# Optimization experiments

Measured on AMD Instinct MI355X. Metric: run time of the kernel, lower is better.

The kernel has to match this reference:

```python
import jax, jax.numpy as jnp
import numpy as np

B, H, N, F = 64, 24, 32, 256

def setup_inputs() -> dict:
    key = jax.random.key(0)
    ks = jax.random.split(key, 6)
    s = 1.0 / np.sqrt(F)
    return {
        "Q": jax.random.normal(ks[0], (B, N, F), jnp.float32),
        "K": jax.random.normal(ks[1], (B, H, N, F), jnp.float32),
        "V": jax.random.normal(ks[2], (B, H, N, F), jnp.float32),
        "Wq": jax.random.normal(ks[3], (N, F, F), jnp.float32) * s,
        "bq": jnp.zeros((N, F), jnp.float32),
        "Wk": jax.random.normal(ks[4], (N, H, F, F), jnp.float32) * s,
        "bk": jnp.zeros((N, H, F), jnp.float32),
        "Wv": jax.random.normal(ks[5], (N, H, F, F), jnp.float32) * s,
        "bv": jnp.zeros((N, H, F), jnp.float32),
    }

def reference(Q, K, V, Wq, bq, Wk, bk, Wv, bv):
    # Per-node query projection: [B,N,F]
    QWq = jnp.einsum('bnf,nfg->bng', Q, Wq) + bq
    # Per-node, per-encoder-step key/value projections: [B,N,H,F]
    KWk = jnp.einsum('bhnf,nhfg->bnhg', K, Wk) + bk
    VWv = jnp.einsum('bhnf,nhfg->bnhg', V, Wv) + bv
    # Attention scores over the H encoder steps (no sqrt(F) scaling, as in source)
    logits = jnp.einsum('bng,bnhg->bnh', QWq, KWk)
    scores = jax.nn.softmax(logits, axis=-1)          # [B,N,H]
    heads = jnp.einsum('bnh,bnhg->bng', scores, VWv)  # [B,N,F]
    return heads, scores
```

## Files before the change

### kernel.cpp

```cpp
#include <hip/hip_runtime.h>

typedef __attribute__((ext_vector_type(8))) short short8;
typedef __attribute__((ext_vector_type(4))) float f32x4;

#define B_ 64
#define H_ 24
#define N_ 32
#define F_ 256

__device__ __forceinline__ float bf2f(unsigned short u) {
    return __uint_as_float(((unsigned)u) << 16);
}
__device__ __forceinline__ unsigned short f2bf(float f) {
    unsigned u = __float_as_uint(f);
    u += 0x7fffu + ((u >> 16) & 1u);
    return (unsigned short)(u >> 16);
}
__device__ __forceinline__ unsigned pack_hi(float f0, float f1) {
    return (__float_as_uint(f0) >> 16) | (__float_as_uint(f1) & 0xffff0000u);
}
__device__ __forceinline__ float res_lo(float f) {
    return f - __uint_as_float(__float_as_uint(f) & 0xffff0000u);
}

struct StageT {
    unsigned short Ah[64 * 32];
    unsigned short Al[64 * 32];
    unsigned short Wh[256 * 32];
    unsigned short Wl[256 * 32];
};
union Smem {
    StageT t;
    unsigned short outT[64 * 256];
};

template<bool SPLIT>
__device__ __forceinline__ void gemm_f32(
    const float* __restrict__ Ab, long rstride,
    const float* __restrict__ Wb, Smem& sm, f32x4 acc[4][4])
{
    const int t    = threadIdx.x;
    const int lane = t & 63;
    const int wv   = t >> 6;
    const int l15  = lane & 15;
    const int quad = lane >> 4;
    const int arow = t >> 2, achk = (t & 3) * 8;
    const float* aSrc = Ab + (long)arow * rstride + achk;
    const float* wSrc = Wb + (long)(wv * 8) * 256 + lane * 4;
    const int pos  = wv ^ (lane & 3);
    const int bpos = quad ^ ((l15 >> 2) & 3);

    union F4 { float4 v; float e[4]; };

    float4 a0 = *(const float4*)(aSrc);
    float4 a1 = *(const float4*)(aSrc + 4);
    F4 r[8];
    #pragma unroll
    for (int i = 0; i < 8; i++) r[i].v = *(const float4*)(wSrc + i * 256);

    #pragma unroll
    for (int ks = 0; ks < 8; ks++) {
        __syncthreads();
        {
            uint4 h;
            h.x = pack_hi(a0.x, a0.y); h.y = pack_hi(a0.z, a0.w);
            h.z = pack_hi(a1.x, a1.y); h.w = pack_hi(a1.z, a1.w);
            *(uint4*)&sm.t.Ah[arow * 32 + achk] = h;
            if (SPLIT) {
                uint4 l;
                l.x = pack_hi(res_lo(a0.x), res_lo(a0.y));
                l.y = pack_hi(res_lo(a0.z), res_lo(a0.w));
                l.z = pack_hi(res_lo(a1.x), res_lo(a1.y));
                l.w = pack_hi(res_lo(a1.z), res_lo(a1.w));
                *(uint4*)&sm.t.Al[arow * 32 + achk] = l;
            }
            #pragma unroll
            for (int j = 0; j < 4; j++) {
                uint4 hh;
                hh.x = pack_hi(r[0].e[j], r[1].e[j]);
                hh.y = pack_hi(r[2].e[j], r[3].e[j]);
                hh.z = pack_hi(r[4].e[j], r[5].e[j]);
                hh.w = pack_hi(r[6].e[j], r[7].e[j]);
                *(uint4*)&sm.t.Wh[(lane * 4 + j) * 32 + pos * 8] = hh;
                if (SPLIT) {
                    uint4 ll;
                    ll.x = pack_hi(res_lo(r[0].e[j]), res_lo(r[1].e[j]));
                    ll.y = pack_hi(res_lo(r[2].e[j]), res_lo(r[3].e[j]));
                    ll.z = pack_hi(res_lo(r[4].e[j]), res_lo(r[5].e[j]));
                    ll.w = pack_hi(res_lo(r[6].e[j]), res_lo(r[7].e[j]));
                    *(uint4*)&sm.t.Wl[(lane * 4 + j) * 32 + pos * 8] = ll;
                }
            }
        }
        __syncthreads();
        float4 na0, na1;
        F4 nr[8];
        if (ks < 7) {
            const int k1 = (ks + 1) * 32;
            na0 = *(const float4*)(aSrc + k1);
            na1 = *(const float4*)(aSrc + k1 + 4);
            #pragma unroll
            for (int i = 0; i < 8; i++)
                nr[i].v = *(const float4*)(wSrc + k1 * 256 + i * 256);
        }
        {
            short8 ah[4];
            #pragma unroll
            for (int mi = 0; mi < 4; mi++)
                ah[mi] = *(const short8*)&sm.t.Ah[(mi * 16 + l15) * 32 + quad * 8];
            if (SPLIT) {
                short8 al[4];
                #pragma unroll
                for (int mi = 0; mi < 4; mi++)
                    al[mi] = *(const short8*)&sm.t.Al[(mi * 16 + l15) * 32 + quad * 8];
                #pragma unroll
                for (int ni = 0; ni < 4; ni++) {
                    int g = wv * 64 + ni * 16 + l15;
                    short8 bh = *(const short8*)&sm.t.Wh[g * 32 + bpos * 8];
                    short8 bl = *(const short8*)&sm.t.Wl[g * 32 + bpos * 8];
                    #pragma unroll
                    for (int mi = 0; mi < 4; mi++) {
                        acc[mi][ni] = __builtin_amdgcn_mfma_f32_16x16x32_bf16(al[mi], bh, acc[mi][ni], 0, 0, 0);
                        acc[mi][ni] = __builtin_amdgcn_mfma_f32_16x16x32_bf16(ah[mi], bl, acc[mi][ni], 0, 0, 0);
                        acc[mi][ni] = __builtin_amdgcn_mfma_f32_16x16x32_bf16(ah[mi], bh, acc[mi][ni], 0, 0, 0);
                    }
                }
            } else {
                #pragma unroll
                for (int ni = 0; ni < 4; ni++) {
                    int g = wv * 64 + ni * 16 + l15;
                    short8 bh = *(const short8*)&sm.t.Wh[g * 32 + bpos * 8];
                    #pragma unroll
                    for (int mi = 0; mi < 4; mi++)
                        acc[mi][ni] = __builtin_amdgcn_mfma_f32_16x16x32_bf16(ah[mi], bh, acc[mi][ni], 0, 0, 0);
                }
            }
        }
        a0 = na0; a1 = na1;
        #pragma unroll
        for (int i = 0; i < 8; i++) r[i] = nr[i];
    }
}

__global__ __launch_bounds__(256, 3) void k_qproj(
    const float* __restrict__ Q, const float* __restrict__ Wq,
    const float* __restrict__ bq, float* __restrict__ qws)
{
    const int n = blockIdx.x;
    __shared__ Smem sm;
    f32x4 acc[4][4];
    #pragma unroll
    for (int i = 0; i < 4; i++)
        #pragma unroll
        for (int j = 0; j < 4; j++) acc[i][j] = (f32x4){0.f, 0.f, 0.f, 0.f};

    gemm_f32<true>(Q + n * F_, (long)(N_ * F_), Wq + (long)n * F_ * F_, sm, acc);

    const int t = threadIdx.x, lane = t & 63, wv = t >> 6;
    const int l15 = lane & 15, quad = lane >> 4;
    const float* bias = bq + n * F_;
    float* dst = qws + (long)n * (B_ * F_);
    #pragma unroll
    for (int ni = 0; ni < 4; ni++) {
        int g = wv * 64 + ni * 16 + l15;
        float bb = bias[g];
        #pragma unroll
        for (int mi = 0; mi < 4; mi++)
            #pragma unroll
            for (int reg = 0; reg < 4; reg++) {
                int r = mi * 16 + quad * 4 + reg;
                dst[r * 256 + g] = acc[mi][ni][reg] + bb;
            }
    }
}

__global__ __launch_bounds__(256, 3) void k_kvproj(
    const float* __restrict__ Kx, const float* __restrict__ Vx,
    const float* __restrict__ Wk, const float* __restrict__ bk,
    const float* __restrict__ Wv, const float* __restrict__ bv,
    const float* __restrict__ qws, float* __restrict__ logits,
    unsigned short* __restrict__ vws)
{
    const int nh = blockIdx.x;
    const int n = nh / H_;
    const int h = nh - n * H_;
    const bool isV = (blockIdx.y != 0);
    const float* X    = isV ? Vx : Kx;
    const float* W    = (isV ? Wv : Wk) + (long)nh * F_ * F_;
    const float* bias = (isV ? bv : bk) + nh * F_;

    __shared__ Smem sm;
    __shared__ float slog[64];
    const int t = threadIdx.x;
    if (!isV && t < 64) slog[t] = 0.f;

    f32x4 acc[4][4];
    #pragma unroll
    for (int i = 0; i < 4; i++)
        #pragma unroll
        for (int j = 0; j < 4; j++) acc[i][j] = (f32x4){0.f, 0.f, 0.f, 0.f};

    const float* Xb = X + (long)(h * N_ + n) * F_;
    if (isV) gemm_f32<false>(Xb, (long)(H_ * N_ * F_), W, sm, acc);
    else     gemm_f32<true >(Xb, (long)(H_ * N_ * F_), W, sm, acc);

    const int lane = t & 63, wv = t >> 6, l15 = lane & 15, quad = lane >> 4;

    if (!isV) {
        const float* qrow = qws + (long)n * (B_ * F_);
        #pragma unroll
        for (int mi = 0; mi < 4; mi++) {
            float p[4] = {0.f, 0.f, 0.f, 0.f};
            #pragma unroll
            for (int ni = 0; ni < 4; ni++) {
                int g = wv * 64 + ni * 16 + l15;
                float bb = bias[g];
                #pragma unroll
                for (int reg = 0; reg < 4; reg++) {
                    int r = mi * 16 + quad * 4 + reg;
                    p[reg] += (acc[mi][ni][reg] + bb) * qrow[r * 256 + g];
                }
            }
            #pragma unroll
            for (int off = 1; off < 16; off <<= 1)
                #pragma unroll
                for (int reg = 0; reg < 4; reg++)
                    p[reg] += __shfl_xor(p[reg], off, 64);
            if (l15 == 0)
                #pragma unroll
                for (int reg = 0; reg < 4; reg++)
                    atomicAdd(&slog[mi * 16 + quad * 4 + reg], p[reg]);
        }
        __syncthreads();
        if (t < 64) logits[(long)nh * 64 + t] = slog[t];
    } else {
        __syncthreads();
        #pragma unroll
        for (int ni = 0; ni < 4; ni++) {
            int g = wv * 64 + ni * 16 + l15;
            float bb = bias[g];
            #pragma unroll
            for (int mi = 0; mi < 4; mi++)
                #pragma unroll
                for (int reg = 0; reg < 4; reg++) {
                    int r = mi * 16 + quad * 4 + reg;
                    sm.outT[r * 256 + g] = f2bf(acc[mi][ni][reg] + bb);
                }
        }
        __syncthreads();
        unsigned short* dst = vws + (long)nh * (B_ * F_);
        #pragma unroll
        for (int it = 0; it < 8; it++) {
            int row = it * 8 + (t >> 5);
            int c = t & 31;
            uint4 v = *(const uint4*)(&sm.outT[row * 256 + c * 8]);
            *(uint4*)(dst + row * 256 + c * 8) = v;
        }
    }
}

__global__ __launch_bounds__(64) void k_attn(
    const float* __restrict__ logits,
    const unsigned short* __restrict__ vws,
    float* __restrict__ out)
{
    const int bx = blockIdx.x;
    const int b = bx >> 5;
    const int n = bx & 31;
    const int t = threadIdx.x;
    __shared__ float sl[24], se[24];
    if (t < 24) sl[t] = logits[(long)(n * H_ + t) * 64 + b];
    __syncthreads();
    float mx = -1e30f;
    #pragma unroll
    for (int h = 0; h < H_; h++) mx = fmaxf(mx, sl[h]);
    if (t < 24) se[t] = expf(sl[t] - mx);
    __syncthreads();
    float den = 0.f;
    #pragma unroll
    for (int h = 0; h < H_; h++) den += se[h];
    float inv = 1.0f / den;
    if (t < 24)
        out[(long)B_ * N_ * F_ + (long)(b * N_ + n) * H_ + t] = se[t] * inv;

    const int g0 = t * 4;
    float hv[4] = {0.f, 0.f, 0.f, 0.f};
    #pragma unroll
    for (int h = 0; h < H_; h++) {
        float s = se[h] * inv;
        const unsigned short* vp = vws + (((long)(n * H_ + h) * 64 + b) << 8) + g0;
        union { uint2 u; unsigned short e[4]; } vv;
        vv.u = *(const uint2*)vp;
        #pragma unroll
        for (int j = 0; j < 4; j++) hv[j] += s * bf2f(vv.e[j]);
    }
    float4 ov = make_float4(hv[0], hv[1], hv[2], hv[3]);
    *(float4*)(out + ((long)b * N_ + n) * F_ + g0) = ov;
}

extern "C" void kernel_launch(void* const* d_in, const int* in_sizes, int n_in,
                              void* d_out, int out_size, void* d_ws, size_t ws_size,
                              hipStream_t stream) {
    const float* Q  = (const float*)d_in[0];
    const float* K  = (const float*)d_in[1];
    const float* V  = (const float*)d_in[2];
    const float* Wq = (const float*)d_in[3];
    const float* bq = (const float*)d_in[4];
    const float* Wk = (const float*)d_in[5];
    const float* bk = (const float*)d_in[6];
    const float* Wv = (const float*)d_in[7];
    const float* bv = (const float*)d_in[8];

    char* ws = (char*)d_ws;
    float* qws          = (float*)ws;
    float* logits       = (float*)(ws + 2097152);
    unsigned short* vws = (unsigned short*)(ws + 2097152 + 262144);

    k_qproj<<<N_, 256, 0, stream>>>(Q, Wq, bq, qws);
    k_kvproj<<<dim3(N_ * H_, 2), 256, 0, stream>>>(K, V, Wk, bk, Wv, bv, qws, logits, vws);
    k_attn<<<B_ * N_, 64, 0, stream>>>(logits, vws, (float*)d_out);
}
```

Before: 496.4 us.

## Split Q projection over K with atomics and restructure GEMM prefetch barriers

The Q projection now launches 8× more blocks, one per 32-wide K-slice, and accumulates partial results into a pre-zeroed workspace with atomicAdd. A separate zeroing kernel runs first. The GEMM loop issues the next global loads before the LDS write stage and replaces __syncthreads with explicit lgkmcnt waits plus s_barrier. It also raises occupancy hints to 4 blocks per CU and reuses shared memory for the logit scratch. The aim is to fix the 32-block underutilization of the Q projection and to overlap global loads with LDS conversion, at the cost of an extra launch, atomic traffic and nondeterministic summation order.

```diff
diff --git a/kernel.cpp b/kernel.cpp
--- a/kernel.cpp
+++ b/kernel.cpp
@@ -37,7 +37,8 @@
 template<bool SPLIT>
 __device__ __forceinline__ void gemm_f32(
     const float* __restrict__ Ab, long rstride,
-    const float* __restrict__ Wb, Smem& sm, f32x4 acc[4][4])
+    const float* __restrict__ Wb, Smem& sm, f32x4 acc[4][4],
+    int ksBeg, int ksEnd)
 {
     const int t    = threadIdx.x;
     const int lane = t & 63;
@@ -52,15 +53,28 @@
 
     union F4 { float4 v; float e[4]; };
 
-    float4 a0 = *(const float4*)(aSrc);
-    float4 a1 = *(const float4*)(aSrc + 4);
+    float4 a0 = *(const float4*)(aSrc + ksBeg * 32);
+    float4 a1 = *(const float4*)(aSrc + ksBeg * 32 + 4);
     F4 r[8];
     #pragma unroll
-    for (int i = 0; i < 8; i++) r[i].v = *(const float4*)(wSrc + i * 256);
-
-    #pragma unroll
-    for (int ks = 0; ks < 8; ks++) {
-        __syncthreads();
+    for (int i = 0; i < 8; i++)
+        r[i].v = *(const float4*)(wSrc + (long)(ksBeg * 32 + i) * 256);
+
+    for (int ks = ksBeg; ks < ksEnd; ks++) {
+        asm volatile("s_waitcnt lgkmcnt(0)" ::: "memory");
+        __builtin_amdgcn_s_barrier();
+
+        float4 na0, na1;
+        F4 nr[8];
+        if (ks + 1 < ksEnd) {
+            const int k1 = (ks + 1) * 32;
+            na0 = *(const float4*)(aSrc + k1);
+            na1 = *(const float4*)(aSrc + k1 + 4);
+            #pragma unroll
+            for (int i = 0; i < 8; i++)
+                nr[i].v = *(const float4*)(wSrc + (long)(k1 + i) * 256);
+        }
+
         {
             uint4 h;
             h.x = pack_hi(a0.x, a0.y); h.y = pack_hi(a0.z, a0.w);
@@ -92,17 +106,9 @@
                 }
             }
         }
-        __syncthreads();
-        float4 na0, na1;
-        F4 nr[8];
-        if (ks < 7) {
-            const int k1 = (ks + 1) * 32;
-            na0 = *(const float4*)(aSrc + k1);
-            na1 = *(const float4*)(aSrc + k1 + 4);
-            #pragma unroll
-            for (int i = 0; i < 8; i++)
-                nr[i].v = *(const float4*)(wSrc + k1 * 256 + i * 256);
-        }
+        asm volatile("s_waitcnt lgkmcnt(0)" ::: "memory");
+        __builtin_amdgcn_s_barrier();
+
         {
             short8 ah[4];
             #pragma unroll
@@ -142,11 +148,16 @@
     }
 }
 
-__global__ __launch_bounds__(256, 3) void k_qproj(
+__global__ __launch_bounds__(256) void k_zero(float4* __restrict__ p) {
+    p[blockIdx.x * 256 + threadIdx.x] = (float4){0.f, 0.f, 0.f, 0.f};
+}
+
+__global__ __launch_bounds__(256, 4) void k_qproj(
     const float* __restrict__ Q, const float* __restrict__ Wq,
     const float* __restrict__ bq, float* __restrict__ qws)
 {
-    const int n = blockIdx.x;
+    const int n  = blockIdx.x;
+    const int ks = blockIdx.y;
     __shared__ Smem sm;
     f32x4 acc[4][4];
     #pragma unroll
@@ -154,7 +165,8 @@
         #pragma unroll
         for (int j = 0; j < 4; j++) acc[i][j] = (f32x4){0.f, 0.f, 0.f, 0.f};
 
-    gemm_f32<true>(Q + n * F_, (long)(N_ * F_), Wq + (long)n * F_ * F_, sm, acc);
+    gemm_f32<true>(Q + n * F_, (long)(N_ * F_), Wq + (long)n * F_ * F_, sm, acc,
+                   ks, ks + 1);
 
     const int t = threadIdx.x, lane = t & 63, wv = t >> 6;
     const int l15 = lane & 15, quad = lane >> 4;
@@ -163,18 +175,18 @@
     #pragma unroll
     for (int ni = 0; ni < 4; ni++) {
         int g = wv * 64 + ni * 16 + l15;
-        float bb = bias[g];
+        float bb = (ks == 0) ? bias[g] : 0.f;
         #pragma unroll
         for (int mi = 0; mi < 4; mi++)
             #pragma unroll
             for (int reg = 0; reg < 4; reg++) {
                 int r = mi * 16 + quad * 4 + reg;
-                dst[r * 256 + g] = acc[mi][ni][reg] + bb;
+                atomicAdd(&dst[r * 256 + g], acc[mi][ni][reg] + bb);
             }
     }
 }
 
-__global__ __launch_bounds__(256, 3) void k_kvproj(
+__global__ __launch_bounds__(256, 4) void k_kvproj(
     const float* __restrict__ Kx, const float* __restrict__ Vx,
     const float* __restrict__ Wk, const float* __restrict__ bk,
     const float* __restrict__ Wv, const float* __restrict__ bv,
@@ -190,9 +202,7 @@
     const float* bias = (isV ? bv : bk) + nh * F_;
 
     __shared__ Smem sm;
-    __shared__ float slog[64];
     const int t = threadIdx.x;
-    if (!isV && t < 64) slog[t] = 0.f;
 
     f32x4 acc[4][4];
     #pragma unroll
@@ -201,12 +211,16 @@
         for (int j = 0; j < 4; j++) acc[i][j] = (f32x4){0.f, 0.f, 0.f, 0.f};
 
     const float* Xb = X + (long)(h * N_ + n) * F_;
-    if (isV) gemm_f32<false>(Xb, (long)(H_ * N_ * F_), W, sm, acc);
-    else     gemm_f32<true >(Xb, (long)(H_ * N_ * F_), W, sm, acc);
+    if (isV) gemm_f32<false>(Xb, (long)(H_ * N_ * F_), W, sm, acc, 0, 8);
+    else     gemm_f32<true >(Xb, (long)(H_ * N_ * F_), W, sm, acc, 0, 8);
 
     const int lane = t & 63, wv = t >> 6, l15 = lane & 15, quad = lane >> 4;
 
     if (!isV) {
+        float* slog = (float*)&sm;
+        __syncthreads();
+        if (t < 64) slog[t] = 0.f;
+        __syncthreads();
         const float* qrow = qws + (long)n * (B_ * F_);
         #pragma unroll
         for (int mi = 0; mi < 4; mi++) {
@@ -316,7 +330,8 @@
     float* logits       = (float*)(ws + 2097152);
     unsigned short* vws = (unsigned short*)(ws + 2097152 + 262144);
 
-    k_qproj<<<N_, 256, 0, stream>>>(Q, Wq, bq, qws);
+    k_zero<<<512, 256, 0, stream>>>((float4*)qws);
+    k_qproj<<<dim3(N_, 8), 256, 0, stream>>>(Q, Wq, bq, qws);
     k_kvproj<<<dim3(N_ * H_, 2), 256, 0, stream>>>(K, V, Wk, bk, Wv, bv, qws, logits, vws);
     k_attn<<<B_ * N_, 64, 0, stream>>>(logits, vws, (float*)d_out);
 }
```

Result: slower. 565.9 us (+14.0%).
